# Kernel tuning notes

Hardware: AMD Instinct MI355X
Metric: run time of the kernel (lower is better)

The kernel has to match this reference:

```python
import jax, jax.numpy as jnp
import numpy as np

N, E = 10000, 320000
C = 64          # channel multiplicity of 0e and 1o node features
A = 4           # node_attrs (species one-hot) dim
NB = 8          # radial basis size (edge_embedding dim)
H = 8           # invariant_neurons
AVG_NEIGH = 32.0
LOG2 = 0.6931471805599453

def ssp(x):
    # ShiftedSoftPlus
    return jax.nn.softplus(x) - LOG2


def setup_inputs() -> dict:
    key = jax.random.key(0)
    ks = jax.random.split(key, 13)
    d = dict(
        node_features=jax.random.normal(ks[0], (N, 4 * C), jnp.float32),   # [N, C + 3C]
        node_attrs=jax.random.normal(ks[1], (N, A), jnp.float32),
        edge_attrs=jax.random.normal(ks[2], (E, 4), jnp.float32),          # sh l=0,1
        edge_embedding=jax.random.uniform(ks[3], (E, NB), jnp.float32),
        edge_index=jax.random.randint(ks[4], (2, E), 0, N),
        # e3nn Linear (internal weights) per-l blocks
        W_lin1_0=jax.random.normal(ks[5], (C, C), jnp.float32),
        W_lin1_1=jax.random.normal(ks[6], (C, C), jnp.float32),
        # radial FullyConnectedNet: NB -> H -> 4C (tp.weight_numel)
        W_fc1=jax.random.normal(ks[7], (NB, H), jnp.float32),
        W_fc2=jax.random.normal(ks[8], (H, 4 * C), jnp.float32),
        # linear_2: irreps_mid.simplify() = 2Cx0e+2Cx1o -> Cx0e+Cx1o
        W_lin2_0=jax.random.normal(ks[9], (2 * C, C), jnp.float32),
        W_lin2_1=jax.random.normal(ks[10], (2 * C, C), jnp.float32),
        # self-connection FullyConnectedTensorProduct weights (node_attrs are scalars)
        W_sc0=jax.random.normal(ks[11], (C, A, C), jnp.float32),
        W_sc1=jax.random.normal(ks[12], (C, A, C), jnp.float32),
    )
    return d


def _forward(node_features, node_attrs, edge_attrs, edge_embedding, edge_index,
             W_lin1_0, W_lin1_1, W_fc1, W_fc2, W_lin2_0, W_lin2_1, W_sc0, W_sc1):
    n = node_features.shape[0]
    e = edge_attrs.shape[0]
    x0 = node_features[:, :C]                      # [N, C]   scalars (0e)
    x1 = node_features[:, C:].reshape(n, C, 3)     # [N, C, 3] vectors (1o)

    # self-connection: FullyConnectedTensorProduct(feat, node_attrs(0e)) -> feat
    sc_norm = 1.0 / np.sqrt(C * A)
    sc0 = jnp.einsum('nu,na,uav->nv', x0, node_attrs, W_sc0) * sc_norm
    sc1 = jnp.einsum('num,na,uav->nvm', x1, node_attrs, W_sc1) * sc_norm

    # linear_1 (per-irrep mixing, e3nn normalization 1/sqrt(fan_in))
    y0 = (x0 @ W_lin1_0) / np.sqrt(C)
    y1 = jnp.einsum('num,uv->nvm', x1, W_lin1_1) / np.sqrt(C)

    # radial MLP -> per-edge TP weights [E, 4C] (instruction order p1..p4)
    h = ssp((edge_embedding @ W_fc1) / np.sqrt(NB))
    w = (h @ W_fc2) / np.sqrt(H)
    wp1, wp2, wp3, wp4 = jnp.split(w, 4, axis=1)   # each [E, C]

    src = edge_index[1]
    dst = edge_index[0]
    xs0 = y0[src]                                  # [E, C]
    xs1 = y1[src]                                  # [E, C, 3]
    sh0 = edge_attrs[:, :1]                        # [E, 1]
    sh1 = edge_attrs[:, 1:4]                       # [E, 3]

    # uvu tensor product paths (component normalization)
    mid_s0 = wp1 * xs0 * sh0                                            # 0e x 0e -> 0e
    mid_s1 = wp4 * jnp.einsum('eum,em->eu', xs1, sh1) / np.sqrt(3.0)    # 1o x 1o -> 0e
    mid_v0 = (wp2 * xs0)[:, :, None] * sh1[:, None, :]                  # 0e x 1o -> 1o
    mid_v1 = wp3[:, :, None] * xs1 * sh0[:, :, None]                    # 1o x 0e -> 1o

    edge_feat = jnp.concatenate(
        [mid_s0, mid_s1, mid_v0.reshape(e, 3 * C), mid_v1.reshape(e, 3 * C)], axis=1
    )                                                                    # [E, 8C]

    # scatter-sum to destination nodes, then divide by sqrt(avg_num_neighbors)
    agg = jnp.zeros((n, 8 * C), edge_feat.dtype).at[dst].add(edge_feat)
    agg = agg / np.sqrt(AVG_NEIGH)

    s = agg[:, :2 * C]                              # [N, 2C] scalars
    v = agg[:, 2 * C:].reshape(n, 2 * C, 3)         # [N, 2C, 3] vectors

    # linear_2 on simplified mid irreps
    o0 = (s @ W_lin2_0) / np.sqrt(2 * C) + sc0
    o1 = jnp.einsum('num,uv->nvm', v, W_lin2_1) / np.sqrt(2 * C) + sc1

    return jnp.concatenate([o0, o1.reshape(n, 3 * C)], axis=1)          # [N, 4C]


def reference(node_features, node_attrs, edge_attrs, edge_embedding, edge_index,
              W_lin1_0, W_lin1_1, W_fc1, W_fc2, W_lin2_0, W_lin2_1, W_sc0, W_sc1):
    return _forward(node_features, node_attrs, edge_attrs, edge_embedding, edge_index,
                    W_lin1_0, W_lin1_1, W_fc1, W_fc2, W_lin2_0, W_lin2_1, W_sc0, W_sc1)
```

## Files before the change

### kernel.cpp

```cpp
#include <hip/hip_runtime.h>


__global__ __launch_bounds__(256) void k_hist(const int* __restrict__ ei,
                                              int* __restrict__ cnt, int nedges) {
  int e = blockIdx.x * 256 + threadIdx.x;
  if (e < nedges) atomicAdd(&cnt[ei[e]], 1);
}

__global__ __launch_bounds__(1024) void k_scan(const int* __restrict__ cnt,
                                               int* __restrict__ offs,
                                               int* __restrict__ cur,
                                               int nnodes, int nedges) {
  __shared__ int s_wtot[16], s_wpre[16];
  const int tid = threadIdx.x;
  const int lane = tid & 63;
  const int w = tid >> 6;
  int vals[16];
  int tot = 0;
  const int start = tid * 16;
#pragma unroll
  for (int k = 0; k < 16; ++k) {
    int i = start + k;
    int c = (i < nnodes) ? cnt[i] : 0;
    vals[k] = c;
    tot += c;
  }
  int incl = tot;
#pragma unroll
  for (int off = 1; off < 64; off <<= 1) {
    int v = __shfl_up(incl, off, 64);
    if (lane >= off) incl += v;
  }
  if (lane == 63) s_wtot[w] = incl;
  __syncthreads();
  if (tid == 0) {
    int run = 0;
#pragma unroll
    for (int i = 0; i < 16; ++i) { s_wpre[i] = run; run += s_wtot[i]; }
  }
  __syncthreads();
  int run = s_wpre[w] + (incl - tot);
#pragma unroll
  for (int k = 0; k < 16; ++k) {
    int i = start + k;
    if (i < nnodes) {
      offs[i] = run;
      cur[i] = run;
      run += vals[k];
    }
  }
  if (tid == 0) offs[nnodes] = nedges;
}

__global__ __launch_bounds__(256) void k_build(
    const int* __restrict__ ei, const float* __restrict__ ee,
    const float* __restrict__ ea, const float* __restrict__ Wf1,
    int* __restrict__ cur, int* __restrict__ srcs,
    float* __restrict__ ehw, int nedges) {
  __shared__ float s_w[64];
  const int tid = threadIdx.x;
  if (tid < 64) s_w[tid] = Wf1[tid];
  __syncthreads();
  int e = blockIdx.x * 256 + tid;
  if (e >= nedges) return;
  const int d = ei[e];
  const int s = ei[nedges + e];
  const int p = atomicAdd(&cur[d], 1);
  srcs[p] = s;
  const float4 a = *(const float4*)(ee + (size_t)e * 8);
  const float4 b = *(const float4*)(ee + (size_t)e * 8 + 4);
  float r[8];
  const float is8 = 0.35355339059327379f;
#pragma unroll
  for (int j = 0; j < 8; ++j) {
    float dd = a.x * s_w[0 * 8 + j] + a.y * s_w[1 * 8 + j] + a.z * s_w[2 * 8 + j] +
               a.w * s_w[3 * 8 + j] + b.x * s_w[4 * 8 + j] + b.y * s_w[5 * 8 + j] +
               b.z * s_w[6 * 8 + j] + b.w * s_w[7 * 8 + j];
    dd *= is8;
    float sp = fmaxf(dd, 0.f) + log1pf(__expf(-fabsf(dd)));
    r[j] = (sp - 0.69314718055994531f) * is8;
  }
  const size_t q = (size_t)p * 12;
  *(float4*)(ehw + q) = make_float4(r[0], r[1], r[2], r[3]);
  *(float4*)(ehw + q + 4) = make_float4(r[4], r[5], r[6], r[7]);
  *(float4*)(ehw + q + 8) = *(const float4*)(ea + (size_t)e * 4);
}

__global__ __launch_bounds__(256) void k_node_pre(
    const float* __restrict__ nf, const float* __restrict__ na,
    const float* __restrict__ W10, const float* __restrict__ W11,
    const float* __restrict__ Ws0, const float* __restrict__ Ws1,
    float* __restrict__ yq, float* __restrict__ out, int nnodes) {
  __shared__ float s_nf[16][256];
  __shared__ float s_na[16][4];
  const int tid = threadIdx.x;
  const int lane = tid & 63;
  const int wv = tid >> 6;
  const int base = blockIdx.x * 16;

  for (int i = tid; i < 16 * 256; i += 256) {
    int r = i >> 8, c = i & 255;
    int n = base + r;
    s_nf[r][c] = (n < nnodes) ? nf[(size_t)n * 256 + c] : 0.f;
  }
  if (tid < 64) {
    int r = tid >> 2, c = tid & 3;
    int n = base + r;
    s_na[r][c] = (n < nnodes) ? na[(size_t)n * 4 + c] : 0.f;
  }
  __syncthreads();

  const int r0 = wv * 4;
  const int v = lane;
  float y0a[4] = {0.f, 0.f, 0.f, 0.f};
  float y1a[4][3] = {};
  float sc0a[4] = {0.f, 0.f, 0.f, 0.f};
  float sc1a[4][3] = {};

#pragma unroll 4
  for (int u = 0; u < 64; ++u) {
    float x0r[4], x1r[4][3];
#pragma unroll
    for (int r = 0; r < 4; ++r) {
      x0r[r] = s_nf[r0 + r][u];
#pragma unroll
      for (int m = 0; m < 3; ++m) x1r[r][m] = s_nf[r0 + r][64 + u * 3 + m];
    }
    const float w0 = W10[u * 64 + v];
    const float w1 = W11[u * 64 + v];
#pragma unroll
    for (int r = 0; r < 4; ++r) {
      y0a[r] = fmaf(x0r[r], w0, y0a[r]);
#pragma unroll
      for (int m = 0; m < 3; ++m) y1a[r][m] = fmaf(x1r[r][m], w1, y1a[r][m]);
    }
#pragma unroll
    for (int a = 0; a < 4; ++a) {
      const float ws0 = Ws0[u * 256 + a * 64 + v];
      const float ws1 = Ws1[u * 256 + a * 64 + v];
#pragma unroll
      for (int r = 0; r < 4; ++r) {
        const float nav = s_na[r0 + r][a];
        sc0a[r] = fmaf(x0r[r] * nav, ws0, sc0a[r]);
        const float t = nav * ws1;
#pragma unroll
        for (int m = 0; m < 3; ++m)
          sc1a[r][m] = fmaf(x1r[r][m], t, sc1a[r][m]);
      }
    }
  }

#pragma unroll
  for (int r = 0; r < 4; ++r) {
    const int n = base + r0 + r;
    if (n < nnodes) {
      *(float4*)(yq + ((size_t)n * 64 + v) * 4) =
          make_float4(y0a[r] * 0.125f, y1a[r][0] * 0.125f,
                      y1a[r][1] * 0.125f, y1a[r][2] * 0.125f);
      out[(size_t)n * 256 + v] = sc0a[r] * 0.0625f;
#pragma unroll
      for (int m = 0; m < 3; ++m)
        out[(size_t)n * 256 + 64 + v * 3 + m] = sc1a[r][m] * 0.0625f;
    }
  }
}

__global__ __launch_bounds__(256, 4) void k_agg(
    const float* __restrict__ yq, const float* __restrict__ ehw,
    const int* __restrict__ srcs, const int* __restrict__ offs,
    const float* __restrict__ Wf2, float* __restrict__ agg, int nnodes) {
  const int tid = threadIdx.x;
  const int u = tid & 63;
  const int wv = tid >> 6;
  const int n = blockIdx.x * 4 + wv;
  if (n >= nnodes) return;

  float wreg[32];
#pragma unroll
  for (int j = 0; j < 8; ++j)
#pragma unroll
    for (int q = 0; q < 4; ++q) wreg[j * 4 + q] = Wf2[j * 256 + q * 64 + u];

  float as0 = 0.f, as1 = 0.f;
  float av0[3] = {0.f, 0.f, 0.f};
  float av1[3] = {0.f, 0.f, 0.f};

  const int beg = offs[n], end = offs[n + 1];
#pragma unroll 4
  for (int i = beg; i < end; ++i) {
    const int src = srcs[i];
    const float4 yv = *(const float4*)(yq + ((size_t)src * 64 + u) * 4);
    const float4 h0 = *(const float4*)(ehw + (size_t)i * 12);
    const float4 h1 = *(const float4*)(ehw + (size_t)i * 12 + 4);
    const float4 sh = *(const float4*)(ehw + (size_t)i * 12 + 8);
    const float hv[8] = {h0.x, h0.y, h0.z, h0.w, h1.x, h1.y, h1.z, h1.w};
    float wp[4] = {0.f, 0.f, 0.f, 0.f};
#pragma unroll
    for (int j = 0; j < 8; ++j)
#pragma unroll
      for (int q = 0; q < 4; ++q) wp[q] = fmaf(hv[j], wreg[j * 4 + q], wp[q]);
    const float dot3 = yv.y * sh.y + yv.z * sh.z + yv.w * sh.w;
    as0 = fmaf(wp[0] * yv.x, sh.x, as0);
    as1 = fmaf(wp[3], dot3, as1);
    const float t2 = wp[1] * yv.x;
    av0[0] = fmaf(t2, sh.y, av0[0]);
    av0[1] = fmaf(t2, sh.z, av0[1]);
    av0[2] = fmaf(t2, sh.w, av0[2]);
    const float t3 = wp[2] * sh.x;
    av1[0] = fmaf(t3, yv.y, av1[0]);
    av1[1] = fmaf(t3, yv.z, av1[1]);
    av1[2] = fmaf(t3, yv.w, av1[2]);
  }

  float* ap = agg + (size_t)n * 512;
  ap[u] = as0;
  ap[64 + u] = as1 * 0.57735026918962576f;
#pragma unroll
  for (int m = 0; m < 3; ++m) {
    ap[128 + m * 64 + u] = av0[m];
    ap[320 + m * 64 + u] = av1[m];
  }
}

__global__ __launch_bounds__(256, 4) void k_lin2(
    const float* __restrict__ agg, const float* __restrict__ W20,
    const float* __restrict__ W21, float* __restrict__ out, int nnodes) {
  __shared__ float s_x[4][4][512];
  const int tid = threadIdx.x;
  const int u = tid & 63;
  const int wv = tid >> 6;
  const int nb = blockIdx.x * 16 + wv * 4;

#pragma unroll
  for (int r = 0; r < 4; ++r) {
    const int n = nb + r;
    if (n < nnodes) {
      const float4* srcp = (const float4*)(agg + (size_t)n * 512);
      float4* dst = (float4*)&s_x[wv][r][0];
      dst[u] = srcp[u];
      dst[64 + u] = srcp[64 + u];
    }
  }

  float o0[4] = {0.f, 0.f, 0.f, 0.f};
  float o1[4][3] = {};

#pragma unroll 2
  for (int up = 0; up < 64; ++up) {
    const float w20a = W20[up * 64 + u];
    const float w20b = W20[(64 + up) * 64 + u];
    const float w21a = W21[up * 64 + u];
    const float w21b = W21[(64 + up) * 64 + u];
#pragma unroll
    for (int r = 0; r < 4; ++r) {
      o0[r] = fmaf(s_x[wv][r][up], w20a, o0[r]);
      o0[r] = fmaf(s_x[wv][r][64 + up], w20b, o0[r]);
#pragma unroll
      for (int m = 0; m < 3; ++m) {
        o1[r][m] = fmaf(s_x[wv][r][128 + m * 64 + up], w21a, o1[r][m]);
        o1[r][m] = fmaf(s_x[wv][r][320 + m * 64 + up], w21b, o1[r][m]);
      }
    }
  }

  const float scl = 1.f / 64.f;
#pragma unroll
  for (int r = 0; r < 4; ++r) {
    const int n = nb + r;
    if (n < nnodes) {
      out[(size_t)n * 256 + u] += o0[r] * scl;
#pragma unroll
      for (int m = 0; m < 3; ++m)
        out[(size_t)n * 256 + 64 + u * 3 + m] += o1[r][m] * scl;
    }
  }
}

extern "C" void kernel_launch(void* const* d_in, const int* in_sizes, int n_in,
                              void* d_out, int out_size, void* d_ws, size_t ws_size,
                              hipStream_t stream) {
  const float* nf = (const float*)d_in[0];
  const float* na = (const float*)d_in[1];
  const float* ea = (const float*)d_in[2];
  const float* ee = (const float*)d_in[3];
  const int* ei = (const int*)d_in[4];
  const float* W10 = (const float*)d_in[5];
  const float* W11 = (const float*)d_in[6];
  const float* Wf1 = (const float*)d_in[7];
  const float* Wf2 = (const float*)d_in[8];
  const float* W20 = (const float*)d_in[9];
  const float* W21 = (const float*)d_in[10];
  const float* Ws0 = (const float*)d_in[11];
  const float* Ws1 = (const float*)d_in[12];
  float* out = (float*)d_out;

  const int N = in_sizes[1] / 4;
  const int E = in_sizes[2] / 4;

  char* w = (char*)d_ws;
  auto carve = [&](size_t bytes) {
    char* p = w;
    w += (bytes + 255) & ~(size_t)255;
    return p;
  };
  float* yq = (float*)carve((size_t)N * 256 * sizeof(float));
  float* ehw = (float*)carve((size_t)E * 12 * sizeof(float));
  float* agg = (float*)carve((size_t)N * 512 * sizeof(float));
  int* cnt = (int*)carve((size_t)N * sizeof(int));
  int* offs = (int*)carve((size_t)(N + 1) * sizeof(int));
  int* cur = (int*)carve((size_t)N * sizeof(int));
  int* srcs = (int*)carve((size_t)E * sizeof(int));

  hipMemsetAsync(cnt, 0, (size_t)N * sizeof(int), stream);
  const int egrid = (E + 255) / 256;
  k_hist<<<egrid, 256, 0, stream>>>(ei, cnt, E);
  k_scan<<<1, 1024, 0, stream>>>(cnt, offs, cur, N, E);
  k_build<<<egrid, 256, 0, stream>>>(ei, ee, ea, Wf1, cur, srcs, ehw, E);
  k_node_pre<<<(N + 15) / 16, 256, 0, stream>>>(nf, na, W10, W11, Ws0, Ws1, yq, out, N);
  k_agg<<<(N + 3) / 4, 256, 0, stream>>>(yq, ehw, srcs, offs, Wf2, agg, N);
  k_lin2<<<(N + 15) / 16, 256, 0, stream>>>(agg, W20, W21, out, N);
}
```

Before: 285.8 us.

## Store intermediates and weights as bf16 to cut memory traffic

Node projections, edge radial weights and the aggregated buffer are now stored as bf16, and weight pairs are packed into 32-bit words by a new pre-pass kernel, so each gather or load moves half the bytes. k_node_pre also shrinks to 128-thread blocks of 8 nodes. The aim is to cut bandwidth in the gather-heavy aggregation and in the weight loads. The cost is reduced precision in the intermediates and the weights, plus one extra kernel launch.

After: 336.0 us. +17.6%, slower.

```diff
diff --git a/kernel.cpp b/kernel.cpp
--- a/kernel.cpp
+++ b/kernel.cpp
@@ -1,5 +1,38 @@
 #include <hip/hip_runtime.h>
 
+
+__device__ __forceinline__ unsigned short f2b(float f) {
+  unsigned u = __float_as_uint(f);
+  return (unsigned short)((u + 0x7FFFu + ((u >> 16) & 1u)) >> 16);
+}
+__device__ __forceinline__ unsigned packb(float a, float b) {
+  return (unsigned)f2b(a) | ((unsigned)f2b(b) << 16);
+}
+__device__ __forceinline__ float blo(unsigned p) { return __uint_as_float(p << 16); }
+__device__ __forceinline__ float bhi(unsigned p) { return __uint_as_float(p & 0xFFFF0000u); }
+__device__ __forceinline__ float b2f(unsigned short h) {
+  return __uint_as_float((unsigned)h << 16);
+}
+
+__global__ __launch_bounds__(256) void k_pack(
+    const float* __restrict__ W10, const float* __restrict__ W11,
+    const float* __restrict__ Ws0, const float* __restrict__ Ws1,
+    const float* __restrict__ W20, const float* __restrict__ W21,
+    unsigned* __restrict__ wpk1, unsigned* __restrict__ wpks,
+    unsigned* __restrict__ wpk2a, unsigned* __restrict__ wpk2b) {
+  int i = blockIdx.x * 256 + threadIdx.x;
+  if (i < 4096) wpk1[i] = packb(W10[i], W11[i]);
+  else if (i < 4096 + 16384) {
+    int j = i - 4096;
+    wpks[j] = packb(Ws0[j], Ws1[j]);
+  } else if (i < 4096 + 16384 + 4096) {
+    int j = i - (4096 + 16384);
+    wpk2a[j] = packb(W20[j], W20[4096 + j]);
+  } else if (i < 4096 + 16384 + 8192) {
+    int j = i - (4096 + 16384 + 4096);
+    wpk2b[j] = packb(W21[j], W21[4096 + j]);
+  }
+}
 
 __global__ __launch_bounds__(256) void k_hist(const int* __restrict__ ei,
                                               int* __restrict__ cnt, int nedges) {
@@ -56,7 +89,7 @@
     const int* __restrict__ ei, const float* __restrict__ ee,
     const float* __restrict__ ea, const float* __restrict__ Wf1,
     int* __restrict__ cur, int* __restrict__ srcs,
-    float* __restrict__ ehw, int nedges) {
+    uint4* __restrict__ ehh, float4* __restrict__ esh, int nedges) {
   __shared__ float s_w[64];
   const int tid = threadIdx.x;
   if (tid < 64) s_w[tid] = Wf1[tid];
@@ -80,30 +113,28 @@
     float sp = fmaxf(dd, 0.f) + log1pf(__expf(-fabsf(dd)));
     r[j] = (sp - 0.69314718055994531f) * is8;
   }
-  const size_t q = (size_t)p * 12;
-  *(float4*)(ehw + q) = make_float4(r[0], r[1], r[2], r[3]);
-  *(float4*)(ehw + q + 4) = make_float4(r[4], r[5], r[6], r[7]);
-  *(float4*)(ehw + q + 8) = *(const float4*)(ea + (size_t)e * 4);
-}
-
-__global__ __launch_bounds__(256) void k_node_pre(
+  ehh[p] = make_uint4(packb(r[0], r[1]), packb(r[2], r[3]),
+                      packb(r[4], r[5]), packb(r[6], r[7]));
+  esh[p] = *(const float4*)(ea + (size_t)e * 4);
+}
+
+__global__ __launch_bounds__(128) void k_node_pre(
     const float* __restrict__ nf, const float* __restrict__ na,
-    const float* __restrict__ W10, const float* __restrict__ W11,
-    const float* __restrict__ Ws0, const float* __restrict__ Ws1,
-    float* __restrict__ yq, float* __restrict__ out, int nnodes) {
-  __shared__ float s_nf[16][256];
-  __shared__ float s_na[16][4];
+    const unsigned* __restrict__ wpk1, const unsigned* __restrict__ wpks,
+    unsigned short* __restrict__ yqb, float* __restrict__ out, int nnodes) {
+  __shared__ float s_nf[8][256];
+  __shared__ float s_na[8][4];
   const int tid = threadIdx.x;
   const int lane = tid & 63;
   const int wv = tid >> 6;
-  const int base = blockIdx.x * 16;
-
-  for (int i = tid; i < 16 * 256; i += 256) {
+  const int base = blockIdx.x * 8;
+
+  for (int i = tid; i < 8 * 256; i += 128) {
     int r = i >> 8, c = i & 255;
     int n = base + r;
     s_nf[r][c] = (n < nnodes) ? nf[(size_t)n * 256 + c] : 0.f;
   }
-  if (tid < 64) {
+  if (tid < 32) {
     int r = tid >> 2, c = tid & 3;
     int n = base + r;
     s_na[r][c] = (n < nnodes) ? na[(size_t)n * 4 + c] : 0.f;
@@ -126,8 +157,9 @@
 #pragma unroll
       for (int m = 0; m < 3; ++m) x1r[r][m] = s_nf[r0 + r][64 + u * 3 + m];
     }
-    const float w0 = W10[u * 64 + v];
-    const float w1 = W11[u * 64 + v];
+    const unsigned q1 = wpk1[u * 64 + v];
+    const float w0 = blo(q1);
+    const float w1 = bhi(q1);
 #pragma unroll
     for (int r = 0; r < 4; ++r) {
       y0a[r] = fmaf(x0r[r], w0, y0a[r]);
@@ -136,8 +168,9 @@
     }
 #pragma unroll
     for (int a = 0; a < 4; ++a) {
-      const float ws0 = Ws0[u * 256 + a * 64 + v];
-      const float ws1 = Ws1[u * 256 + a * 64 + v];
+      const unsigned qs = wpks[(u * 4 + a) * 64 + v];
+      const float ws0 = blo(qs);
+      const float ws1 = bhi(qs);
 #pragma unroll
       for (int r = 0; r < 4; ++r) {
         const float nav = s_na[r0 + r][a];
@@ -154,9 +187,12 @@
   for (int r = 0; r < 4; ++r) {
     const int n = base + r0 + r;
     if (n < nnodes) {
-      *(float4*)(yq + ((size_t)n * 64 + v) * 4) =
-          make_float4(y0a[r] * 0.125f, y1a[r][0] * 0.125f,
-                      y1a[r][1] * 0.125f, y1a[r][2] * 0.125f);
+      ushort4 yv;
+      yv.x = f2b(y0a[r] * 0.125f);
+      yv.y = f2b(y1a[r][0] * 0.125f);
+      yv.z = f2b(y1a[r][1] * 0.125f);
+      yv.w = f2b(y1a[r][2] * 0.125f);
+      *(ushort4*)(yqb + ((size_t)n * 64 + v) * 4) = yv;
       out[(size_t)n * 256 + v] = sc0a[r] * 0.0625f;
 #pragma unroll
       for (int m = 0; m < 3; ++m)
@@ -166,9 +202,10 @@
 }
 
 __global__ __launch_bounds__(256, 4) void k_agg(
-    const float* __restrict__ yq, const float* __restrict__ ehw,
-    const int* __restrict__ srcs, const int* __restrict__ offs,
-    const float* __restrict__ Wf2, float* __restrict__ agg, int nnodes) {
+    const unsigned short* __restrict__ yqb, const uint4* __restrict__ ehh,
+    const float4* __restrict__ esh, const int* __restrict__ srcs,
+    const int* __restrict__ offs, const float* __restrict__ Wf2,
+    unsigned short* __restrict__ aggb, int nnodes) {
   const int tid = threadIdx.x;
   const int u = tid & 63;
   const int wv = tid >> 6;
@@ -189,42 +226,43 @@
 #pragma unroll 4
   for (int i = beg; i < end; ++i) {
     const int src = srcs[i];
-    const float4 yv = *(const float4*)(yq + ((size_t)src * 64 + u) * 4);
-    const float4 h0 = *(const float4*)(ehw + (size_t)i * 12);
-    const float4 h1 = *(const float4*)(ehw + (size_t)i * 12 + 4);
-    const float4 sh = *(const float4*)(ehw + (size_t)i * 12 + 8);
-    const float hv[8] = {h0.x, h0.y, h0.z, h0.w, h1.x, h1.y, h1.z, h1.w};
+    const ushort4 yb = *(const ushort4*)(yqb + ((size_t)src * 64 + u) * 4);
+    const uint4 hp = ehh[i];
+    const float4 sh = esh[i];
+    const float hv[8] = {blo(hp.x), bhi(hp.x), blo(hp.y), bhi(hp.y),
+                         blo(hp.z), bhi(hp.z), blo(hp.w), bhi(hp.w)};
     float wp[4] = {0.f, 0.f, 0.f, 0.f};
 #pragma unroll
     for (int j = 0; j < 8; ++j)
 #pragma unroll
       for (int q = 0; q < 4; ++q) wp[q] = fmaf(hv[j], wreg[j * 4 + q], wp[q]);
-    const float dot3 = yv.y * sh.y + yv.z * sh.z + yv.w * sh.w;
-    as0 = fmaf(wp[0] * yv.x, sh.x, as0);
+    const float y0 = b2f(yb.x), y1 = b2f(yb.y), y2 = b2f(yb.z), y3 = b2f(yb.w);
+    const float dot3 = y1 * sh.y + y2 * sh.z + y3 * sh.w;
+    as0 = fmaf(wp[0] * y0, sh.x, as0);
     as1 = fmaf(wp[3], dot3, as1);
-    const float t2 = wp[1] * yv.x;
+    const float t2 = wp[1] * y0;
     av0[0] = fmaf(t2, sh.y, av0[0]);
     av0[1] = fmaf(t2, sh.z, av0[1]);
     av0[2] = fmaf(t2, sh.w, av0[2]);
     const float t3 = wp[2] * sh.x;
-    av1[0] = fmaf(t3, yv.y, av1[0]);
-    av1[1] = fmaf(t3, yv.z, av1[1]);
-    av1[2] = fmaf(t3, yv.w, av1[2]);
-  }
-
-  float* ap = agg + (size_t)n * 512;
-  ap[u] = as0;
-  ap[64 + u] = as1 * 0.57735026918962576f;
+    av1[0] = fmaf(t3, y1, av1[0]);
+    av1[1] = fmaf(t3, y2, av1[1]);
+    av1[2] = fmaf(t3, y3, av1[2]);
+  }
+
+  unsigned short* ap = aggb + (size_t)n * 512;
+  ap[u] = f2b(as0);
+  ap[64 + u] = f2b(as1 * 0.57735026918962576f);
 #pragma unroll
   for (int m = 0; m < 3; ++m) {
-    ap[128 + m * 64 + u] = av0[m];
-    ap[320 + m * 64 + u] = av1[m];
+    ap[128 + m * 64 + u] = f2b(av0[m]);
+    ap[320 + m * 64 + u] = f2b(av1[m]);
   }
 }
 
 __global__ __launch_bounds__(256, 4) void k_lin2(
-    const float* __restrict__ agg, const float* __restrict__ W20,
-    const float* __restrict__ W21, float* __restrict__ out, int nnodes) {
+    const unsigned short* __restrict__ aggb, const unsigned* __restrict__ wpk2a,
+    const unsigned* __restrict__ wpk2b, float* __restrict__ out, int nnodes) {
   __shared__ float s_x[4][4][512];
   const int tid = threadIdx.x;
   const int u = tid & 63;
@@ -235,10 +273,10 @@
   for (int r = 0; r < 4; ++r) {
     const int n = nb + r;
     if (n < nnodes) {
-      const float4* srcp = (const float4*)(agg + (size_t)n * 512);
-      float4* dst = (float4*)&s_x[wv][r][0];
-      dst[u] = srcp[u];
-      dst[64 + u] = srcp[64 + u];
+      const uint4 aw = *(const uint4*)(aggb + (size_t)n * 512 + u * 8);
+      float4* dst = (float4*)&s_x[wv][r][u * 8];
+      dst[0] = make_float4(blo(aw.x), bhi(aw.x), blo(aw.y), bhi(aw.y));
+      dst[1] = make_float4(blo(aw.z), bhi(aw.z), blo(aw.w), bhi(aw.w));
     }
   }
 
@@ -247,10 +285,10 @@
 
 #pragma unroll 2
   for (int up = 0; up < 64; ++up) {
-    const float w20a = W20[up * 64 + u];
-    const float w20b = W20[(64 + up) * 64 + u];
-    const float w21a = W21[up * 64 + u];
-    const float w21b = W21[(64 + up) * 64 + u];
+    const unsigned qa = wpk2a[up * 64 + u];
+    const unsigned qb = wpk2b[up * 64 + u];
+    const float w20a = blo(qa), w20b = bhi(qa);
+    const float w21a = blo(qb), w21b = bhi(qb);
 #pragma unroll
     for (int r = 0; r < 4; ++r) {
       o0[r] = fmaf(s_x[wv][r][up], w20a, o0[r]);
@@ -303,20 +341,27 @@
     w += (bytes + 255) & ~(size_t)255;
     return p;
   };
-  float* yq = (float*)carve((size_t)N * 256 * sizeof(float));
-  float* ehw = (float*)carve((size_t)E * 12 * sizeof(float));
-  float* agg = (float*)carve((size_t)N * 512 * sizeof(float));
+  unsigned short* yqb = (unsigned short*)carve((size_t)N * 256 * 2);
+  uint4* ehh = (uint4*)carve((size_t)E * 16);
+  float4* esh = (float4*)carve((size_t)E * 16);
+  unsigned short* aggb = (unsigned short*)carve((size_t)N * 512 * 2);
+  unsigned* wpk1 = (unsigned*)carve(4096 * 4);
+  unsigned* wpks = (unsigned*)carve(16384 * 4);
+  unsigned* wpk2a = (unsigned*)carve(4096 * 4);
+  unsigned* wpk2b = (unsigned*)carve(4096 * 4);
   int* cnt = (int*)carve((size_t)N * sizeof(int));
   int* offs = (int*)carve((size_t)(N + 1) * sizeof(int));
   int* cur = (int*)carve((size_t)N * sizeof(int));
   int* srcs = (int*)carve((size_t)E * sizeof(int));
 
   hipMemsetAsync(cnt, 0, (size_t)N * sizeof(int), stream);
+  k_pack<<<(4096 + 16384 + 8192 + 255) / 256, 256, 0, stream>>>(
+      W10, W11, Ws0, Ws1, W20, W21, wpk1, wpks, wpk2a, wpk2b);
   const int egrid = (E + 255) / 256;
   k_hist<<<egrid, 256, 0, stream>>>(ei, cnt, E);
   k_scan<<<1, 1024, 0, stream>>>(cnt, offs, cur, N, E);
-  k_build<<<egrid, 256, 0, stream>>>(ei, ee, ea, Wf1, cur, srcs, ehw, E);
-  k_node_pre<<<(N + 15) / 16, 256, 0, stream>>>(nf, na, W10, W11, Ws0, Ws1, yq, out, N);
-  k_agg<<<(N + 3) / 4, 256, 0, stream>>>(yq, ehw, srcs, offs, Wf2, agg, N);
-  k_lin2<<<(N + 15) / 16, 256, 0, stream>>>(agg, W20, W21, out, N);
-}
+  k_build<<<egrid, 256, 0, stream>>>(ei, ee, ea, Wf1, cur, srcs, ehh, esh, E);
+  k_node_pre<<<(N + 7) / 8, 128, 0, stream>>>(nf, na, wpk1, wpks, yqb, out, N);
+  k_agg<<<(N + 3) / 4, 256, 0, stream>>>(yqb, ehh, esh, srcs, offs, Wf2, aggb, N);
+  k_lin2<<<(N + 15) / 16, 256, 0, stream>>>(aggb, wpk2a, wpk2b, out, N);
+}
```
